# Kernel optimization log

Measured on AMD Instinct MI355X. Metric: run time of the kernel, lower is better.

The kernel has to match this reference:

```python
import jax, jax.numpy as jnp
import numpy as np

TAU = 0.5  # temperature from init_kwargs


def _semi_loss(h1, h2):
    # GRACE-style InfoNCE: -log( e^{sim(i,i')/tau} / (sum_refl + sum_between - e^{sim(i,i)/tau}) )
    n1 = h1 / jnp.linalg.norm(h1, axis=1, keepdims=True)
    n2 = h2 / jnp.linalg.norm(h2, axis=1, keepdims=True)
    refl = jnp.exp((n1 @ n1.T) / TAU)   # [N, N]
    betw = jnp.exp((n1 @ n2.T) / TAU)   # [N, N]
    denom = refl.sum(axis=1) + betw.sum(axis=1) - jnp.diagonal(refl)
    return -jnp.log(jnp.diagonal(betw) / denom)


def _contrast(h1, h2):
    # forward_v1 with batch_size=0 (batched path is mathematically identical)
    return (0.5 * (_semi_loss(h1, h2) + _semi_loss(h2, h1))).mean()


def _proj(z, Wa, ba, Wb, bb):
    # fc_b(elu(fc_a(z))); torch Linear: y = x @ W.T + b
    return jax.nn.elu(z @ Wa.T + ba) @ Wb.T + bb


def setup_inputs() -> dict:
    key = jax.random.key(0)
    ks = jax.random.split(key, 11)
    N, A, B = 8192, 32, 32
    D = A * B
    s = 1.0 / np.sqrt(D)
    inp = {
        'ta': jax.random.normal(ks[0], (N, A, B), dtype=jnp.float32),
        'tb': jax.random.normal(ks[1], (N, A, B), dtype=jnp.float32),
        'W1': jax.random.uniform(ks[2], (D, D), jnp.float32, -s, s),
        'b1': jax.random.uniform(ks[3], (D,), jnp.float32, -s, s),
        'W2': jax.random.uniform(ks[4], (D, D), jnp.float32, -s, s),
        'b2': jax.random.uniform(ks[5], (D,), jnp.float32, -s, s),
        'W3': jax.random.uniform(ks[6], (D, D), jnp.float32, -s, s),
        'b3': jax.random.uniform(ks[7], (D,), jnp.float32, -s, s),
        'W4': jax.random.uniform(ks[8], (D, D), jnp.float32, -s, s),
        'b4': jax.random.uniform(ks[9], (D,), jnp.float32, -s, s),
        'w_r1': jnp.array([0.5], dtype=jnp.float32),
    }
    return inp


def reference(ta, tb, W1, b1, W2, b2, W3, b3, W4, b4, w_r1):
    N = ta.shape[0]
    # row view: [N, A*B]
    z1 = ta.reshape(N, -1)
    z2 = tb.reshape(N, -1)
    loss_row = _contrast(_proj(z1, W1, b1, W2, b2), _proj(z2, W1, b1, W2, b2))
    # column view: permute(0,2,1) then flatten -> [N, B*A]
    z1c = jnp.transpose(ta, (0, 2, 1)).reshape(N, -1)
    z2c = jnp.transpose(tb, (0, 2, 1)).reshape(N, -1)
    loss_col = _contrast(_proj(z1c, W3, b3, W4, b4), _proj(z2c, W3, b3, W4, b4))
    w_row = jnp.clip(w_r1[0], 0.0, 1.0)
    return w_row * loss_row + (1.0 - w_row) * loss_col
```

## Files before the change

### kernel.cpp

```cpp
#include <hip/hip_runtime.h>
#include <stdint.h>


typedef unsigned short u16;
typedef __attribute__((ext_vector_type(8))) __bf16 bf16x8;
typedef __attribute__((ext_vector_type(4))) float f32x4;
typedef __attribute__((ext_vector_type(16))) float f32x16;

#define NS 8192
#define DD 1024

__device__ __forceinline__ float bf2f(u16 u) {
    union { uint32_t i; float f; } v; v.i = ((uint32_t)u) << 16; return v.f;
}
__device__ __forceinline__ u16 f2bf(float f) {
    union { float f; uint32_t i; } v; v.f = f;
    return (u16)((v.i + 0x7FFFu + ((v.i >> 16) & 1u)) >> 16);
}

__device__ __forceinline__ void gload16(const u16* g, u16* l) {
    __builtin_amdgcn_global_load_lds(
        (__attribute__((address_space(1))) void*)(uintptr_t)(g),
        (__attribute__((address_space(3))) void*)(uintptr_t)(l), 16, 0, 0);
}


__global__ __launch_bounds__(256) void conv_f2bf(const float* __restrict__ src,
                                                 u16* __restrict__ dst) {
    int i = (blockIdx.x * 256 + threadIdx.x) * 4;
    float4 v = *(const float4*)(src + i);
    ushort4 o;
    o.x = f2bf(v.x); o.y = f2bf(v.y); o.z = f2bf(v.z); o.w = f2bf(v.w);
    *(ushort4*)(dst + i) = o;
}

__global__ __launch_bounds__(256) void conv_cat(const float* __restrict__ a,
                                                const float* __restrict__ b,
                                                u16* __restrict__ Z) {
    size_t i = (size_t)(blockIdx.x * 256 + threadIdx.x) * 4;
    const size_t half = (size_t)NS * DD;
    const float* s = (i < half) ? (a + i) : (b + (i - half));
    float4 v = *(const float4*)s;
    ushort4 o;
    o.x = f2bf(v.x); o.y = f2bf(v.y); o.z = f2bf(v.z); o.w = f2bf(v.w);
    *(ushort4*)(Z + i) = o;
}

__global__ __launch_bounds__(256) void conv_col(const float* __restrict__ a,
                                                const float* __restrict__ b,
                                                u16* __restrict__ Z) {
    size_t i = (size_t)(blockIdx.x * 256 + threadIdx.x) * 4;
    const size_t half = (size_t)NS * DD;
    const float* src; size_t o;
    if (i < half) { src = a; o = i; } else { src = b; o = i - half; }
    size_t row = o >> 10;
    int j = (int)(o & 1023);
    int aI = j & 31, bI = j >> 5;
    const float* rp = src + (row << 10);
    ushort4 ov;
    ov.x = f2bf(rp[aI * 32 + bI]);
    ov.y = f2bf(rp[(aI + 1) * 32 + bI]);
    ov.z = f2bf(rp[(aI + 2) * 32 + bI]);
    ov.w = f2bf(rp[(aI + 3) * 32 + bI]);
    *(ushort4*)(Z + i) = ov;
}

template <int MODE>
__global__ __launch_bounds__(256) void gemm_bt(const u16* A, const u16* B,
                                               const float* __restrict__ bias,
                                               u16* __restrict__ out) {
    __shared__ alignas(16) u16 As[128 * 32];
    __shared__ alignas(16) u16 Bs[128 * 32];
    const int tid = threadIdx.x;

    const int tm = blockIdx.y, tn = blockIdx.x;
    const size_t tileM = (size_t)tm * 128;
    const size_t tileN = (size_t)tn * 128;

    const int csw = ((tid & 3) ^ ((tid >> 4) & 3)) * 8;
    const u16* gA0 = A + (tileM + (tid >> 2)) * DD + csw;
    const u16* gA1 = gA0 + (size_t)64 * DD;
    const u16* gB0 = B + (tileN + (tid >> 2)) * DD + csw;
    const u16* gB1 = gB0 + (size_t)64 * DD;
    u16* lA0 = &As[tid * 8]; u16* lA1 = lA0 + 2048;
    u16* lB0 = &Bs[tid * 8]; u16* lB1 = lB0 + 2048;

    const int lane = tid & 63;
    const int wv = tid >> 6;
    const int wr = (wv >> 1) << 6;
    const int wc = (wv & 1) << 6;
    const int lr = lane & 15;
    const int lh = lane >> 4;
    const int sw = lh ^ ((lr >> 2) & 3);

    const u16* aBase = &As[(wr + lr) * 32 + sw * 8];
    const u16* bBase = &Bs[(wc + lr) * 32 + sw * 8];

    f32x4 acc[4][4];
#pragma unroll
    for (int i = 0; i < 4; i++)
#pragma unroll
        for (int j = 0; j < 4; j++) acc[i][j] = (f32x4)0.0f;

    for (int k0 = 0; k0 < DD; k0 += 32) {
        gload16(gA0 + k0, lA0);
        gload16(gA1 + k0, lA1);
        gload16(gB0 + k0, lB0);
        gload16(gB1 + k0, lB1);
        __syncthreads();
        bf16x8 af[4], bfr[4];
#pragma unroll
        for (int rt = 0; rt < 4; rt++) af[rt] = *(const bf16x8*)(aBase + rt * 512);
#pragma unroll
        for (int ct = 0; ct < 4; ct++) bfr[ct] = *(const bf16x8*)(bBase + ct * 512);
#pragma unroll
        for (int rt = 0; rt < 4; rt++)
#pragma unroll
            for (int ct = 0; ct < 4; ct++)
                acc[rt][ct] = __builtin_amdgcn_mfma_f32_16x16x32_bf16(
                    af[rt], bfr[ct], acc[rt][ct], 0, 0, 0);
        __syncthreads();
    }

    float bcol[4];
#pragma unroll
    for (int ct = 0; ct < 4; ct++) bcol[ct] = bias[tileN + wc + ct * 16 + lr];
#pragma unroll
    for (int rt = 0; rt < 4; rt++) {
#pragma unroll
        for (int r = 0; r < 4; r++) {
            size_t row = tileM + wr + rt * 16 + lh * 4 + r;
            u16* orow = out + row * DD + tileN + wc + lr;
#pragma unroll
            for (int ct = 0; ct < 4; ct++) {
                float v = acc[rt][ct][r] + bcol[ct];
                if (MODE == 0) v = v > 0.0f ? v : expm1f(v);
                orow[ct * 16] = f2bf(v);
            }
        }
    }
}

__global__ __launch_bounds__(256, 3) void gram128(const u16* __restrict__ H,
                                                  float* __restrict__ S) {
    __shared__ alignas(16) u16 As[128 * 32];
    __shared__ alignas(16) u16 Bs[128 * 32];
    const int tid = threadIdx.x;

    int x = blockIdx.x, y = blockIdx.y;
    int tm, tn;
    if (y + x < 128) { tm = y;       tn = y + x; }
    else             { tm = 127 - y; tn = x - 1; }
    const size_t rowA = (size_t)tm * 128;
    const size_t rowB = (size_t)tn * 128;

    const int csw = ((tid & 3) ^ ((tid >> 4) & 3)) * 8;
    const u16* gA0 = H + (rowA + (tid >> 2)) * DD + csw;
    const u16* gA1 = gA0 + (size_t)64 * DD;
    const u16* gB0 = H + (rowB + (tid >> 2)) * DD + csw;
    const u16* gB1 = gB0 + (size_t)64 * DD;
    u16* lA0 = &As[tid * 8]; u16* lA1 = lA0 + 2048;
    u16* lB0 = &Bs[tid * 8]; u16* lB1 = lB0 + 2048;

    const int lane = tid & 63;
    const int wv = tid >> 6;
    const int wr = (wv >> 1) * 64;
    const int wc = (wv & 1) * 64;
    const int c31 = lane & 31;
    const int hi  = lane >> 5;
    const int q4  = (c31 >> 2) & 3;
    const int o0  = (hi ^ q4) * 8;
    const int o1  = o0 ^ 16;
    const int aB = (wr + c31) * 32;
    const int bB = (wc + c31) * 32;

    f32x16 acc[2][2];
#pragma unroll
    for (int i = 0; i < 2; ++i)
#pragma unroll
        for (int j = 0; j < 2; ++j) acc[i][j] = (f32x16)0.0f;

    for (int k0 = 0; k0 < DD; k0 += 32) {
        gload16(gA0 + k0, lA0);
        gload16(gA1 + k0, lA1);
        gload16(gB0 + k0, lB0);
        gload16(gB1 + k0, lB1);
        __syncthreads();
        bf16x8 aF[2][2], bF[2][2];
#pragma unroll
        for (int mt = 0; mt < 2; ++mt) {
            aF[mt][0] = *(const bf16x8*)(&As[aB + mt * 1024 + o0]);
            aF[mt][1] = *(const bf16x8*)(&As[aB + mt * 1024 + o1]);
        }
#pragma unroll
        for (int nt = 0; nt < 2; ++nt) {
            bF[nt][0] = *(const bf16x8*)(&Bs[bB + nt * 1024 + o0]);
            bF[nt][1] = *(const bf16x8*)(&Bs[bB + nt * 1024 + o1]);
        }
#pragma unroll
        for (int mt = 0; mt < 2; ++mt)
#pragma unroll
            for (int nt = 0; nt < 2; ++nt)
#pragma unroll
                for (int kk = 0; kk < 2; ++kk)
                    acc[mt][nt] = __builtin_amdgcn_mfma_f32_32x32x16_bf16(
                        aF[mt][kk], bF[nt][kk], acc[mt][nt], 0, 0, 0);
        __syncthreads();
    }

    const bool offdiag = (tm != tn);
    float csum[2] = {0.f, 0.f};
#pragma unroll
    for (int mt = 0; mt < 2; ++mt) {
#pragma unroll
        for (int j = 0; j < 16; ++j) {
            float rs = 0.0f;
#pragma unroll
            for (int nt = 0; nt < 2; ++nt) {
                float e = __expf(2.0f * acc[mt][nt][j]);
                rs += e;
                csum[nt] += e;
            }
            rs += __shfl_xor(rs, 1);
            rs += __shfl_xor(rs, 2);
            rs += __shfl_xor(rs, 4);
            rs += __shfl_xor(rs, 8);
            rs += __shfl_xor(rs, 16);
            if (c31 == 0) {
                size_t row = rowA + wr + mt * 32 + (j & 3) + 8 * (j >> 2) + 4 * hi;
                atomicAdd(&S[row], rs);
            }
        }
    }
    if (offdiag) {
#pragma unroll
        for (int nt = 0; nt < 2; ++nt) {
            float cs = csum[nt];
            cs += __shfl_xor(cs, 32);
            if (hi == 0) {
                size_t col = rowB + wc + nt * 32 + c31;
                atomicAdd(&S[col], cs);
            }
        }
    }
}

__global__ __launch_bounds__(256) void normalize_kernel(u16* M) {
    __shared__ float red[4];
    const int tid = threadIdx.x;
    u16* row = M + ((size_t)blockIdx.x << 10);
    ushort4 v = ((const ushort4*)row)[tid];
    float x0 = bf2f(v.x), x1 = bf2f(v.y), x2 = bf2f(v.z), x3 = bf2f(v.w);
    float s = x0 * x0 + x1 * x1 + x2 * x2 + x3 * x3;
#pragma unroll
    for (int m = 1; m < 64; m <<= 1) s += __shfl_xor(s, m);
    if ((tid & 63) == 0) red[tid >> 6] = s;
    __syncthreads();
    float inv = rsqrtf(red[0] + red[1] + red[2] + red[3]);
    ushort4 o;
    o.x = f2bf(x0 * inv); o.y = f2bf(x1 * inv);
    o.z = f2bf(x2 * inv); o.w = f2bf(x3 * inv);
    ((ushort4*)row)[tid] = o;
}

__global__ __launch_bounds__(256) void diag_kernel(const u16* M, float* g12) {
    __shared__ float red[4];
    const int tid = threadIdx.x;
    const u16* r1 = M + ((size_t)blockIdx.x << 10);
    const u16* r2 = r1 + ((size_t)NS << 10);
    ushort4 a = ((const ushort4*)r1)[tid];
    ushort4 b = ((const ushort4*)r2)[tid];
    float s = bf2f(a.x) * bf2f(b.x) + bf2f(a.y) * bf2f(b.y) +
              bf2f(a.z) * bf2f(b.z) + bf2f(a.w) * bf2f(b.w);
#pragma unroll
    for (int m = 1; m < 64; m <<= 1) s += __shfl_xor(s, m);
    if ((tid & 63) == 0) red[tid >> 6] = s;
    __syncthreads();
    if (tid == 0) g12[blockIdx.x] = red[0] + red[1] + red[2] + red[3];
}

__global__ __launch_bounds__(256) void final_kernel(const float* Sr, const float* Sc,
                                                    const float* gr, const float* gc,
                                                    const float* w_r1, float* out) {
    __shared__ float red[16];
    const float E2 = 7.389056098930650f;
    float a = 0.f, b = 0.f, c = 0.f, d = 0.f;
    for (int i = threadIdx.x; i < 2 * NS; i += 256) {
        a += logf(Sr[i] - E2);
        b += logf(Sc[i] - E2);
    }
    for (int i = threadIdx.x; i < NS; i += 256) {
        c += gr[i];
        d += gc[i];
    }
#pragma unroll
    for (int m = 1; m < 64; m <<= 1) {
        a += __shfl_xor(a, m); b += __shfl_xor(b, m);
        c += __shfl_xor(c, m); d += __shfl_xor(d, m);
    }
    int w = threadIdx.x >> 6;
    if ((threadIdx.x & 63) == 0) {
        red[w] = a; red[4 + w] = b; red[8 + w] = c; red[12 + w] = d;
    }
    __syncthreads();
    if (threadIdx.x == 0) {
        a = red[0] + red[1] + red[2] + red[3];
        b = red[4] + red[5] + red[6] + red[7];
        c = red[8] + red[9] + red[10] + red[11];
        d = red[12] + red[13] + red[14] + red[15];
        float lr = a / (2.0f * NS) - 2.0f * c / NS;
        float lc = b / (2.0f * NS) - 2.0f * d / NS;
        float w0 = w_r1[0];
        w0 = fminf(fmaxf(w0, 0.0f), 1.0f);
        out[0] = w0 * lr + (1.0f - w0) * lc;
    }
}

extern "C" void kernel_launch(void* const* d_in, const int* in_sizes, int n_in,
                              void* d_out, int out_size, void* d_ws, size_t ws_size,
                              hipStream_t stream) {
    const float* ta = (const float*)d_in[0];
    const float* tb = (const float*)d_in[1];
    const float* W1 = (const float*)d_in[2];
    const float* b1 = (const float*)d_in[3];
    const float* W2 = (const float*)d_in[4];
    const float* b2 = (const float*)d_in[5];
    const float* W3 = (const float*)d_in[6];
    const float* b3 = (const float*)d_in[7];
    const float* W4 = (const float*)d_in[8];
    const float* b4 = (const float*)d_in[9];
    const float* wr = (const float*)d_in[10];
    float* out = (float*)d_out;

    char* p = (char*)d_ws;
    const size_t MAT = (size_t)2 * NS * DD * sizeof(u16);
    u16* Z = (u16*)p;  p += MAT;
    u16* T = (u16*)p;  p += MAT;
    u16* H = (u16*)p;  p += MAT;
    u16* Wb = (u16*)p; p += (size_t)4 * DD * DD * sizeof(u16);
    float* Sr = (float*)p;  p += 2 * NS * sizeof(float);
    float* Sc = (float*)p;  p += 2 * NS * sizeof(float);
    float* gr = (float*)p;  p += NS * sizeof(float);
    float* gc = (float*)p;  p += NS * sizeof(float);

    u16* Wb1 = Wb;
    u16* Wb2 = Wb + (size_t)DD * DD;
    u16* Wb3 = Wb + (size_t)2 * DD * DD;
    u16* Wb4 = Wb + (size_t)3 * DD * DD;

    conv_f2bf<<<1024, 256, 0, stream>>>(W1, Wb1);
    conv_f2bf<<<1024, 256, 0, stream>>>(W2, Wb2);
    conv_f2bf<<<1024, 256, 0, stream>>>(W3, Wb3);
    conv_f2bf<<<1024, 256, 0, stream>>>(W4, Wb4);
    hipMemsetAsync(Sr, 0, 4 * NS * sizeof(float), stream);

    conv_cat<<<16384, 256, 0, stream>>>(ta, tb, Z);
    gemm_bt<0><<<dim3(8, 128), 256, 0, stream>>>(Z, Wb1, b1, T);
    gemm_bt<1><<<dim3(8, 128), 256, 0, stream>>>(T, Wb2, b2, H);
    normalize_kernel<<<16384, 256, 0, stream>>>(H);
    diag_kernel<<<8192, 256, 0, stream>>>(H, gr);
    gram128<<<dim3(129, 64), 256, 0, stream>>>(H, Sr);

    conv_col<<<16384, 256, 0, stream>>>(ta, tb, Z);
    gemm_bt<0><<<dim3(8, 128), 256, 0, stream>>>(Z, Wb3, b3, T);
    gemm_bt<1><<<dim3(8, 128), 256, 0, stream>>>(T, Wb4, b4, H);
    normalize_kernel<<<16384, 256, 0, stream>>>(H);
    diag_kernel<<<8192, 256, 0, stream>>>(H, gc);
    gram128<<<dim3(129, 64), 256, 0, stream>>>(H, Sc);

    final_kernel<<<1, 256, 0, stream>>>(Sr, Sc, gr, gc, wr, out);
}
```

Before: 1.299 ms.

## Load gram MFMA fragments directly from global memory, dropping LDS staging

```diff
diff --git a/kernel.cpp b/kernel.cpp
--- a/kernel.cpp
+++ b/kernel.cpp
@@ -141,10 +141,8 @@
     }
 }
 
-__global__ __launch_bounds__(256, 3) void gram128(const u16* __restrict__ H,
+__global__ __launch_bounds__(256, 4) void gram128(const u16* __restrict__ H,
                                                   float* __restrict__ S) {
-    __shared__ alignas(16) u16 As[128 * 32];
-    __shared__ alignas(16) u16 Bs[128 * 32];
     const int tid = threadIdx.x;
 
     int x = blockIdx.x, y = blockIdx.y;
@@ -154,25 +152,15 @@
     const size_t rowA = (size_t)tm * 128;
     const size_t rowB = (size_t)tn * 128;
 
-    const int csw = ((tid & 3) ^ ((tid >> 4) & 3)) * 8;
-    const u16* gA0 = H + (rowA + (tid >> 2)) * DD + csw;
-    const u16* gA1 = gA0 + (size_t)64 * DD;
-    const u16* gB0 = H + (rowB + (tid >> 2)) * DD + csw;
-    const u16* gB1 = gB0 + (size_t)64 * DD;
-    u16* lA0 = &As[tid * 8]; u16* lA1 = lA0 + 2048;
-    u16* lB0 = &Bs[tid * 8]; u16* lB1 = lB0 + 2048;
-
     const int lane = tid & 63;
     const int wv = tid >> 6;
     const int wr = (wv >> 1) * 64;
     const int wc = (wv & 1) * 64;
     const int c31 = lane & 31;
     const int hi  = lane >> 5;
-    const int q4  = (c31 >> 2) & 3;
-    const int o0  = (hi ^ q4) * 8;
-    const int o1  = o0 ^ 16;
-    const int aB = (wr + c31) * 32;
-    const int bB = (wc + c31) * 32;
+
+    const u16* pA = H + (rowA + wr + c31) * (size_t)DD + hi * 8;
+    const u16* pB = H + (rowB + wc + c31) * (size_t)DD + hi * 8;
 
     f32x16 acc[2][2];
 #pragma unroll
@@ -181,22 +169,14 @@
         for (int j = 0; j < 2; ++j) acc[i][j] = (f32x16)0.0f;
 
     for (int k0 = 0; k0 < DD; k0 += 32) {
-        gload16(gA0 + k0, lA0);
-        gload16(gA1 + k0, lA1);
-        gload16(gB0 + k0, lB0);
-        gload16(gB1 + k0, lB1);
-        __syncthreads();
-        bf16x8 aF[2][2], bF[2][2];
-#pragma unroll
-        for (int mt = 0; mt < 2; ++mt) {
-            aF[mt][0] = *(const bf16x8*)(&As[aB + mt * 1024 + o0]);
-            aF[mt][1] = *(const bf16x8*)(&As[aB + mt * 1024 + o1]);
-        }
-#pragma unroll
-        for (int nt = 0; nt < 2; ++nt) {
-            bF[nt][0] = *(const bf16x8*)(&Bs[bB + nt * 1024 + o0]);
-            bF[nt][1] = *(const bf16x8*)(&Bs[bB + nt * 1024 + o1]);
-        }
+        bf16x8 fA[2][2], fB[2][2];
+#pragma unroll
+        for (int mt = 0; mt < 2; ++mt)
+#pragma unroll
+            for (int kk = 0; kk < 2; ++kk) {
+                fA[mt][kk] = *(const bf16x8*)(pA + (size_t)mt * 32 * DD + k0 + kk * 16);
+                fB[mt][kk] = *(const bf16x8*)(pB + (size_t)mt * 32 * DD + k0 + kk * 16);
+            }
 #pragma unroll
         for (int mt = 0; mt < 2; ++mt)
 #pragma unroll
@@ -204,8 +184,7 @@
 #pragma unroll
                 for (int kk = 0; kk < 2; ++kk)
                     acc[mt][nt] = __builtin_amdgcn_mfma_f32_32x32x16_bf16(
-                        aF[mt][kk], bF[nt][kk], acc[mt][nt], 0, 0, 0);
-        __syncthreads();
+                        fA[mt][kk], fB[nt][kk], acc[mt][nt], 0, 0, 0);
     }
 
     const bool offdiag = (tm != tn);
```

Result: slower. 2.520 ms (+94.0%).
